# Kernel optimization log

Measured on AMD Instinct MI355X. Metric: run time of the kernel, lower is better.

The kernel has to match this reference:

```python
import jax, jax.numpy as jnp
import numpy as np

MEM, W, K = 65536, 128, 8
R = K + 1  # sparse reads + last-used slot
B, IN = 32, 512
IFACE = 2 * W + R + 1  # 266


def setup_inputs() -> dict:
    key = jax.random.key(0)
    ks = jax.random.split(key, 8)
    return {
        "x": jax.random.normal(ks[0], (B, IN), jnp.float32),
        "W_if": jax.random.normal(ks[1], (IN, IFACE), jnp.float32) * 0.02,
        "b_if": jnp.zeros((IFACE,), jnp.float32),
        "memory": jax.random.normal(ks[2], (B, MEM, W), jnp.float32),
        "read_weights": jax.random.uniform(ks[3], (B, 1, R), jnp.float32),
        "read_vectors": jax.random.normal(ks[4], (B, R, W), jnp.float32),
        "read_positions": jax.random.randint(ks[5], (B, R), 0, MEM, jnp.int32),
        "last_used_mem": jax.random.randint(ks[6], (B, 1), 0, MEM, jnp.int32),
    }


def reference(x, W_if, b_if, memory, read_weights, read_vectors, read_positions, last_used_mem):
    b = x.shape[0]
    # interface projection (independent_linears=False path)
    xi = x @ W_if + b_if                                   # (b, 2w+r+1)
    read_query = xi[:, :W]                                  # (b, w)
    write_vector = xi[:, W:2 * W][:, None, :]               # (b, 1, w)
    gate = jax.nn.sigmoid(xi[:, 2 * W:2 * W + R])[:, None, :]  # (b, 1, r)
    write_gate = jax.nn.sigmoid(xi[:, -1])[:, None, None]   # (b, 1, 1)
    # write: interpolate read weights, outer-product update of read vectors
    write_weights = write_gate * (gate * read_weights + (1.0 - gate))  # (b,1,r)
    new_rv = read_vectors + jnp.einsum('bkr,bkw->brw', write_weights, write_vector)  # (b,r,w)
    # write_into_sparse_memory: scatter read vectors into previous read positions
    brange = jnp.arange(b)[:, None]
    memory = memory.at[brange, read_positions].set(new_rv)
    # read: exact KNN (replaces CPU KD-tree search): squared L2 to all cells
    d2 = (jnp.sum(memory * memory, axis=-1)
          - 2.0 * jnp.einsum('bmw,bw->bm', memory, read_query)
          + jnp.sum(read_query * read_query, axis=-1, keepdims=True))  # (b, m)
    _, pos = jax.lax.top_k(-d2, K)                          # K nearest positions
    positions = jnp.concatenate([jnp.clip(pos, 0, MEM - 1), last_used_mem], axis=1)  # (b, r)
    gathered = jnp.take_along_axis(memory, positions[:, :, None], axis=1)  # (b, r, w)
    return gathered[:, :-1, :]  # (b, K, w) — forward output of read()
```

## Files before the change

### kernel.cpp

```cpp
#include <hip/hip_runtime.h>
#include <float.h>
#include <limits.h>

#define MEMN 65536
#define WD 128
#define KSEL 8
#define RD 9
#define BD 32
#define IND 512
#define IFACE 266
#define XI_STRIDE 272

#define KSEG 8
#define KSEG_LEN (IND / KSEG)

#define NCHUNK 64
#define ROWS_PER_CHUNK 1024
#define CAND_SCAN (NCHUNK * KSEL)
#define CAND_REAL (CAND_SCAN + RD)
#define CAND_PER_BATCH 528

typedef float fvec4 __attribute__((ext_vector_type(4)));

#define TOP8_INSERT(bv, bi, vin, iin)                                  \
  { float _v = (vin); int _i = (iin);                                  \
    _Pragma("unroll")                                                  \
    for (int _j = 0; _j < 8; ++_j) {                                   \
      bool _b = (_v < bv[_j]) || (_v == bv[_j] && _i < bi[_j]);        \
      float _tv = bv[_j]; int _ti = bi[_j];                            \
      bv[_j] = _b ? _v : _tv;  bi[_j] = _b ? _i : _ti;                 \
      _v = _b ? _tv : _v;      _i = _b ? _ti : _i;                     \
    } }

__device__ __forceinline__ fvec4 ntload(const void* p) {
  return __builtin_nontemporal_load((const fvec4*)p);
}

__global__ __launch_bounds__(288)
void xi_part_kernel(const float* __restrict__ x, const float* __restrict__ Wif,
                    float* __restrict__ xi_part) {
  const int b = blockIdx.x, seg = blockIdx.y, c = threadIdx.x;
  if (c >= IFACE) return;
  const float* xr = x + b * IND + seg * KSEG_LEN;
  const float* wp = Wif + (size_t)(seg * KSEG_LEN) * IFACE + c;
  float a0 = 0.f, a1 = 0.f, a2 = 0.f, a3 = 0.f;
  #pragma unroll
  for (int k = 0; k < KSEG_LEN; k += 4) {
    a0 += xr[k]     * wp[(size_t)k * IFACE];
    a1 += xr[k + 1] * wp[(size_t)(k + 1) * IFACE];
    a2 += xr[k + 2] * wp[(size_t)(k + 2) * IFACE];
    a3 += xr[k + 3] * wp[(size_t)(k + 3) * IFACE];
  }
  xi_part[(b * KSEG + seg) * XI_STRIDE + c] = (a0 + a1) + (a2 + a3);
}

__global__ __launch_bounds__(320)
void head_kernel(const float* __restrict__ xi_part, const float* __restrict__ bif,
                 const float* __restrict__ read_weights, const float* __restrict__ read_vectors,
                 const int* __restrict__ rpos,
                 float* __restrict__ xi, float* __restrict__ new_rv,
                 float* __restrict__ cand_val, int* __restrict__ cand_idx) {
  const int b = blockIdx.x, t = threadIdx.x;
  __shared__ float xiS[IFACE];
  __shared__ float wwS[RD];
  __shared__ float nvS[RD][WD];

  if (t < IFACE) {
    float acc = bif[t];
    #pragma unroll
    for (int s = 0; s < KSEG; ++s)
      acc += xi_part[(b * KSEG + s) * XI_STRIDE + t];
    xiS[t] = acc;
    xi[b * XI_STRIDE + t] = acc;
  }
  __syncthreads();

  if (t < RD) {
    float g  = 1.f / (1.f + __expf(-xiS[2 * WD + t]));
    float wg = 1.f / (1.f + __expf(-xiS[IFACE - 1]));
    wwS[t] = wg * (g * read_weights[b * RD + t] + (1.f - g));
  }
  __syncthreads();

  if (t < WD) {
    const float wv = xiS[WD + t];
    #pragma unroll
    for (int r = 0; r < RD; ++r) {
      float nv = read_vectors[(b * RD + r) * WD + t] + wwS[r] * wv;
      nvS[r][t] = nv;
      new_rv[(b * RD + r) * WD + t] = nv;
    }
  }
  __syncthreads();

  if (t < 64) {
    const int lane = t;
    const float q0 = xiS[lane * 2], q1 = xiS[lane * 2 + 1];
    for (int r = 0; r < RD; ++r) {
      float m0 = nvS[r][lane * 2], m1 = nvS[r][lane * 2 + 1];
      float s = m0 * (m0 - 2.f * q0) + m1 * (m1 - 2.f * q1);
      #pragma unroll
      for (int off = 32; off; off >>= 1) s += __shfl_xor(s, off);
      if (lane == 0) {
        int p = rpos[b * RD + r];
        bool dup = false;
        for (int r2 = r + 1; r2 < RD; ++r2) dup |= (rpos[b * RD + r2] == p);
        int slot = b * CAND_PER_BATCH + CAND_SCAN + r;
        cand_val[slot] = dup ? FLT_MAX : s;
        cand_idx[slot] = dup ? INT_MAX : p;
      }
    }
  }
}

__global__ __launch_bounds__(256)
void scan_kernel(const float* __restrict__ memory, const float* __restrict__ xi,
                 const int* __restrict__ rpos,
                 float* __restrict__ cand_val, int* __restrict__ cand_idx) {
  const int b = blockIdx.y, chunk = blockIdx.x;
  const int t = threadIdx.x;
  const int w = t >> 6, l = t & 63, g = l >> 2, ln = l & 3;
  const int chunkBase = chunk * ROWS_PER_CHUNK;

  int rp[RD];
  #pragma unroll
  for (int r = 0; r < RD; ++r) rp[r] = rpos[b * RD + r];

  fvec4 tq[8];
  #pragma unroll
  for (int j = 0; j < 8; ++j) {
    fvec4 q = *(const fvec4*)(xi + b * XI_STRIDE + j * 16 + ln * 4);
    tq[j] = q * 2.f;
  }

  float bv[8]; int bi[8];
  #pragma unroll
  for (int j = 0; j < 8; ++j) { bv[j] = FLT_MAX; bi[j] = INT_MAX; }

  const char* memB = (const char*)memory + (size_t)b * MEMN * (WD * 4);

  #pragma unroll 2
  for (int i = 0; i < ROWS_PER_CHUNK / 64; ++i) {
    const int m = chunkBase + i * 64 + w * 16 + g;
    const char* p = memB + (size_t)m * (WD * 4) + ln * 16;
    float sA = 0.f, sB = 0.f;
    #pragma unroll
    for (int j = 0; j < 8; j += 2) {
      fvec4 m0 = ntload(p + j * 64);
      fvec4 m1 = ntload(p + (j + 1) * 64);
      sA += m0.x * (m0.x - tq[j].x) + m0.y * (m0.y - tq[j].y)
          + m0.z * (m0.z - tq[j].z) + m0.w * (m0.w - tq[j].w);
      sB += m1.x * (m1.x - tq[j + 1].x) + m1.y * (m1.y - tq[j + 1].y)
          + m1.z * (m1.z - tq[j + 1].z) + m1.w * (m1.w - tq[j + 1].w);
    }
    float s = sA + sB;
    s += __shfl_xor(s, 1);
    s += __shfl_xor(s, 2);
    if (ln == 0) {
      bool skip = false;
      #pragma unroll
      for (int r = 0; r < RD; ++r) skip |= (m == rp[r]);
      if (!skip && (s < bv[7] || (s == bv[7] && m < bi[7]))) TOP8_INSERT(bv, bi, s, m);
    }
  }

  __shared__ float lv[64][8];
  __shared__ int   li[64][8];
  if (ln == 0) {
    #pragma unroll
    for (int j = 0; j < 8; ++j) { lv[w * 16 + g][j] = bv[j]; li[w * 16 + g][j] = bi[j]; }
  }
  __syncthreads();
  for (int s = 32; s >= 1; s >>= 1) {
    if (t < s) {
      float mv[8]; int mi[8];
      #pragma unroll
      for (int j = 0; j < 8; ++j) { mv[j] = lv[t][j]; mi[j] = li[t][j]; }
      #pragma unroll
      for (int j = 0; j < 8; ++j) {
        float v = lv[t + s][j]; int i = li[t + s][j];
        if (v < mv[7] || (v == mv[7] && i < mi[7])) TOP8_INSERT(mv, mi, v, i);
      }
      #pragma unroll
      for (int j = 0; j < 8; ++j) { lv[t][j] = mv[j]; li[t][j] = mi[j]; }
    }
    __syncthreads();
  }
  if (t < 8) {
    cand_val[b * CAND_PER_BATCH + chunk * 8 + t] = lv[0][t];
    cand_idx[b * CAND_PER_BATCH + chunk * 8 + t] = li[0][t];
  }
}

__global__ __launch_bounds__(128)
void final_kernel(const float* __restrict__ cand_val, const int* __restrict__ cand_idx,
                  const float* __restrict__ memory, const float* __restrict__ new_rv,
                  const int* __restrict__ rpos, float* __restrict__ out) {
  const int b = blockIdx.x, t = threadIdx.x;
  __shared__ float lv[128][8];
  __shared__ int   li[128][8];
  __shared__ int   posS[KSEL], srcS[KSEL];

  float bv[8]; int bi[8];
  #pragma unroll
  for (int j = 0; j < 8; ++j) { bv[j] = FLT_MAX; bi[j] = INT_MAX; }

  for (int e = t; e < CAND_REAL; e += 128) {
    float v = cand_val[b * CAND_PER_BATCH + e];
    int   i = cand_idx[b * CAND_PER_BATCH + e];
    if (v < bv[7] || (v == bv[7] && i < bi[7])) TOP8_INSERT(bv, bi, v, i);
  }
  #pragma unroll
  for (int j = 0; j < 8; ++j) { lv[t][j] = bv[j]; li[t][j] = bi[j]; }
  __syncthreads();

  for (int stride = 64; stride >= 1; stride >>= 1) {
    if (t < stride) {
      #pragma unroll
      for (int j = 0; j < 8; ++j) {
        float v = lv[t + stride][j]; int i = li[t + stride][j];
        if (v < bv[7] || (v == bv[7] && i < bi[7])) TOP8_INSERT(bv, bi, v, i);
      }
      #pragma unroll
      for (int j = 0; j < 8; ++j) { lv[t][j] = bv[j]; li[t][j] = bi[j]; }
    }
    __syncthreads();
  }

  if (t < KSEL) {
    int p = li[0][t];
    int src = -1;
    for (int r = 0; r < RD; ++r) if (rpos[b * RD + r] == p) src = r;
    posS[t] = p; srcS[t] = src;
  }
  __syncthreads();

  for (int e = t; e < KSEL * WD; e += 128) {
    int k = e >> 7, w = e & 127;
    int p = posS[k], src = srcS[k];
    float val = (src >= 0) ? new_rv[(b * RD + src) * WD + w]
                           : memory[((size_t)b * MEMN + p) * WD + w];
    out[b * KSEL * WD + e] = val;
  }
}

extern "C" void kernel_launch(void* const* d_in, const int* in_sizes, int n_in,
                              void* d_out, int out_size, void* d_ws, size_t ws_size,
                              hipStream_t stream) {
  const float* x      = (const float*)d_in[0];
  const float* Wif    = (const float*)d_in[1];
  const float* bif    = (const float*)d_in[2];
  const float* memory = (const float*)d_in[3];
  const float* rw     = (const float*)d_in[4];
  const float* rv     = (const float*)d_in[5];
  const int*   rpos   = (const int*)d_in[6];

  float* ws       = (float*)d_ws;
  float* xi_part  = ws;
  float* xi       = xi_part + BD * KSEG * XI_STRIDE;
  float* new_rv   = xi + BD * XI_STRIDE;
  float* cand_val = new_rv + BD * RD * WD;
  int*   cand_idx = (int*)(cand_val + BD * CAND_PER_BATCH);
  float* out      = (float*)d_out;

  xi_part_kernel<<<dim3(BD, KSEG), dim3(288), 0, stream>>>(x, Wif, xi_part);
  head_kernel<<<dim3(BD), dim3(320), 0, stream>>>(xi_part, bif, rw, rv, rpos,
                                                  xi, new_rv, cand_val, cand_idx);
  scan_kernel<<<dim3(NCHUNK, BD), dim3(256), 0, stream>>>(memory, xi, rpos, cand_val, cand_idx);
  final_kernel<<<dim3(BD), dim3(128), 0, stream>>>(cand_val, cand_idx, memory, new_rv, rpos, out);
}
```

Baseline: 241.7 us.

## Fuse interface projection into head kernel and remap scan to half-wave rows

The separate xi_part kernel is removed, and the x·W_if projection now runs inside head_kernel, split across two 272-thread halves. This drops one launch and a global round trip. The scan kernel changes from 4 lanes per row to 32 lanes per row, with each half-wave reading one contiguous 512-byte row. Each thread holds 4 rows per iteration, and the shared-memory top-8 merge shrinks from 64 to 8 partial lists. Nontemporal loads are replaced with plain loads, and the head projection now runs on only 32 blocks, which limits its parallelism.

```diff
diff --git a/kernel.cpp b/kernel.cpp
--- a/kernel.cpp
+++ b/kernel.cpp
@@ -10,9 +10,6 @@
 #define IND 512
 #define IFACE 266
 #define XI_STRIDE 272
-
-#define KSEG 8
-#define KSEG_LEN (IND / KSEG)
 
 #define NCHUNK 64
 #define ROWS_PER_CHUNK 1024
@@ -32,44 +29,37 @@
       _v = _b ? _tv : _v;      _i = _b ? _ti : _i;                     \
     } }
 
-__device__ __forceinline__ fvec4 ntload(const void* p) {
-  return __builtin_nontemporal_load((const fvec4*)p);
-}
-
-__global__ __launch_bounds__(288)
-void xi_part_kernel(const float* __restrict__ x, const float* __restrict__ Wif,
-                    float* __restrict__ xi_part) {
-  const int b = blockIdx.x, seg = blockIdx.y, c = threadIdx.x;
-  if (c >= IFACE) return;
-  const float* xr = x + b * IND + seg * KSEG_LEN;
-  const float* wp = Wif + (size_t)(seg * KSEG_LEN) * IFACE + c;
-  float a0 = 0.f, a1 = 0.f, a2 = 0.f, a3 = 0.f;
-  #pragma unroll
-  for (int k = 0; k < KSEG_LEN; k += 4) {
-    a0 += xr[k]     * wp[(size_t)k * IFACE];
-    a1 += xr[k + 1] * wp[(size_t)(k + 1) * IFACE];
-    a2 += xr[k + 2] * wp[(size_t)(k + 2) * IFACE];
-    a3 += xr[k + 3] * wp[(size_t)(k + 3) * IFACE];
-  }
-  xi_part[(b * KSEG + seg) * XI_STRIDE + c] = (a0 + a1) + (a2 + a3);
-}
-
-__global__ __launch_bounds__(320)
-void head_kernel(const float* __restrict__ xi_part, const float* __restrict__ bif,
+__global__ __launch_bounds__(544)
+void head_kernel(const float* __restrict__ x, const float* __restrict__ Wif,
+                 const float* __restrict__ bif,
                  const float* __restrict__ read_weights, const float* __restrict__ read_vectors,
                  const int* __restrict__ rpos,
                  float* __restrict__ xi, float* __restrict__ new_rv,
                  float* __restrict__ cand_val, int* __restrict__ cand_idx) {
   const int b = blockIdx.x, t = threadIdx.x;
+  __shared__ float part[2][272];
   __shared__ float xiS[IFACE];
   __shared__ float wwS[RD];
   __shared__ float nvS[RD][WD];
 
+  const int c = t % 272, h = t / 272;
+  if (c < IFACE) {
+    const float* xr = x + b * IND + h * 256;
+    const float* wp = Wif + (size_t)(h * 256) * IFACE + c;
+    float a0 = 0.f, a1 = 0.f, a2 = 0.f, a3 = 0.f;
+    #pragma unroll 4
+    for (int k = 0; k < 256; k += 4) {
+      a0 += xr[k]     * wp[(k)     * IFACE];
+      a1 += xr[k + 1] * wp[(k + 1) * IFACE];
+      a2 += xr[k + 2] * wp[(k + 2) * IFACE];
+      a3 += xr[k + 3] * wp[(k + 3) * IFACE];
+    }
+    part[h][c] = (a0 + a1) + (a2 + a3);
+  }
+  __syncthreads();
+
   if (t < IFACE) {
-    float acc = bif[t];
-    #pragma unroll
-    for (int s = 0; s < KSEG; ++s)
-      acc += xi_part[(b * KSEG + s) * XI_STRIDE + t];
+    float acc = bif[t] + part[0][t] + part[1][t];
     xiS[t] = acc;
     xi[b * XI_STRIDE + t] = acc;
   }
@@ -119,59 +109,68 @@
                  float* __restrict__ cand_val, int* __restrict__ cand_idx) {
   const int b = blockIdx.y, chunk = blockIdx.x;
   const int t = threadIdx.x;
-  const int w = t >> 6, l = t & 63, g = l >> 2, ln = l & 3;
-  const int chunkBase = chunk * ROWS_PER_CHUNK;
+  const int w = t >> 6, l = t & 63;
+  const int half = l >> 5;
+  const int waveBase = chunk * ROWS_PER_CHUNK + w * (ROWS_PER_CHUNK / 4);
 
   int rp[RD];
   #pragma unroll
   for (int r = 0; r < RD; ++r) rp[r] = rpos[b * RD + r];
 
-  fvec4 tq[8];
-  #pragma unroll
-  for (int j = 0; j < 8; ++j) {
-    fvec4 q = *(const fvec4*)(xi + b * XI_STRIDE + j * 16 + ln * 4);
-    tq[j] = q * 2.f;
-  }
+  const fvec4 q = *(const fvec4*)(xi + b * XI_STRIDE + (l & 31) * 4);
+  const fvec4 tq = q * 2.f;
 
   float bv[8]; int bi[8];
   #pragma unroll
   for (int j = 0; j < 8; ++j) { bv[j] = FLT_MAX; bi[j] = INT_MAX; }
 
-  const char* memB = (const char*)memory + (size_t)b * MEMN * (WD * 4);
+  const char* base = (const char*)memory
+                   + ((size_t)b * MEMN + waveBase) * (WD * 4) + (size_t)l * 16;
 
   #pragma unroll 2
-  for (int i = 0; i < ROWS_PER_CHUNK / 64; ++i) {
-    const int m = chunkBase + i * 64 + w * 16 + g;
-    const char* p = memB + (size_t)m * (WD * 4) + ln * 16;
-    float sA = 0.f, sB = 0.f;
+  for (int i = 0; i < 32; ++i) {
+    const char* p = base + (size_t)i * 4096;
+    const fvec4 m0 = *(const fvec4*)(p);
+    const fvec4 m1 = *(const fvec4*)(p + 1024);
+    const fvec4 m2 = *(const fvec4*)(p + 2048);
+    const fvec4 m3 = *(const fvec4*)(p + 3072);
+
+    float s0 = m0.x*(m0.x-tq.x) + m0.y*(m0.y-tq.y) + m0.z*(m0.z-tq.z) + m0.w*(m0.w-tq.w);
+    float s1 = m1.x*(m1.x-tq.x) + m1.y*(m1.y-tq.y) + m1.z*(m1.z-tq.z) + m1.w*(m1.w-tq.w);
+    float s2 = m2.x*(m2.x-tq.x) + m2.y*(m2.y-tq.y) + m2.z*(m2.z-tq.z) + m2.w*(m2.w-tq.w);
+    float s3 = m3.x*(m3.x-tq.x) + m3.y*(m3.y-tq.y) + m3.z*(m3.z-tq.z) + m3.w*(m3.w-tq.w);
+
     #pragma unroll
-    for (int j = 0; j < 8; j += 2) {
-      fvec4 m0 = ntload(p + j * 64);
-      fvec4 m1 = ntload(p + (j + 1) * 64);
-      sA += m0.x * (m0.x - tq[j].x) + m0.y * (m0.y - tq[j].y)
-          + m0.z * (m0.z - tq[j].z) + m0.w * (m0.w - tq[j].w);
-      sB += m1.x * (m1.x - tq[j + 1].x) + m1.y * (m1.y - tq[j + 1].y)
-          + m1.z * (m1.z - tq[j + 1].z) + m1.w * (m1.w - tq[j + 1].w);
-    }
-    float s = sA + sB;
-    s += __shfl_xor(s, 1);
-    s += __shfl_xor(s, 2);
-    if (ln == 0) {
-      bool skip = false;
-      #pragma unroll
-      for (int r = 0; r < RD; ++r) skip |= (m == rp[r]);
-      if (!skip && (s < bv[7] || (s == bv[7] && m < bi[7]))) TOP8_INSERT(bv, bi, s, m);
-    }
-  }
-
-  __shared__ float lv[64][8];
-  __shared__ int   li[64][8];
-  if (ln == 0) {
+    for (int off = 1; off < 32; off <<= 1) {
+      s0 += __shfl_xor(s0, off);
+      s1 += __shfl_xor(s1, off);
+      s2 += __shfl_xor(s2, off);
+      s3 += __shfl_xor(s3, off);
+    }
+
+    if ((l & 31) == 0) {
+      const int mr = waveBase + i * 8 + half;
+      bool k0 = false, k1 = false, k2 = false, k3 = false;
+      #pragma unroll
+      for (int r = 0; r < RD; ++r) {
+        k0 |= (mr     == rp[r]); k1 |= (mr + 2 == rp[r]);
+        k2 |= (mr + 4 == rp[r]); k3 |= (mr + 6 == rp[r]);
+      }
+      if (!k0 && (s0 < bv[7] || (s0 == bv[7] && mr     < bi[7]))) TOP8_INSERT(bv, bi, s0, mr);
+      if (!k1 && (s1 < bv[7] || (s1 == bv[7] && mr + 2 < bi[7]))) TOP8_INSERT(bv, bi, s1, mr + 2);
+      if (!k2 && (s2 < bv[7] || (s2 == bv[7] && mr + 4 < bi[7]))) TOP8_INSERT(bv, bi, s2, mr + 4);
+      if (!k3 && (s3 < bv[7] || (s3 == bv[7] && mr + 6 < bi[7]))) TOP8_INSERT(bv, bi, s3, mr + 6);
+    }
+  }
+
+  __shared__ float lv[8][8];
+  __shared__ int   li[8][8];
+  if ((l & 31) == 0) {
     #pragma unroll
-    for (int j = 0; j < 8; ++j) { lv[w * 16 + g][j] = bv[j]; li[w * 16 + g][j] = bi[j]; }
-  }
-  __syncthreads();
-  for (int s = 32; s >= 1; s >>= 1) {
+    for (int j = 0; j < 8; ++j) { lv[w * 2 + half][j] = bv[j]; li[w * 2 + half][j] = bi[j]; }
+  }
+  __syncthreads();
+  for (int s = 4; s >= 1; s >>= 1) {
     if (t < s) {
       float mv[8]; int mi[8];
       #pragma unroll
@@ -236,10 +235,10 @@
   __syncthreads();
 
   for (int e = t; e < KSEL * WD; e += 128) {
-    int k = e >> 7, w = e & 127;
+    int k = e >> 7, wv = e & 127;
     int p = posS[k], src = srcS[k];
-    float val = (src >= 0) ? new_rv[(b * RD + src) * WD + w]
-                           : memory[((size_t)b * MEMN + p) * WD + w];
+    float val = (src >= 0) ? new_rv[(b * RD + src) * WD + wv]
+                           : memory[((size_t)b * MEMN + p) * WD + wv];
     out[b * KSEL * WD + e] = val;
   }
 }
@@ -256,15 +255,13 @@
   const int*   rpos   = (const int*)d_in[6];
 
   float* ws       = (float*)d_ws;
-  float* xi_part  = ws;
-  float* xi       = xi_part + BD * KSEG * XI_STRIDE;
+  float* xi       = ws;
   float* new_rv   = xi + BD * XI_STRIDE;
   float* cand_val = new_rv + BD * RD * WD;
   int*   cand_idx = (int*)(cand_val + BD * CAND_PER_BATCH);
   float* out      = (float*)d_out;
 
-  xi_part_kernel<<<dim3(BD, KSEG), dim3(288), 0, stream>>>(x, Wif, xi_part);
-  head_kernel<<<dim3(BD), dim3(320), 0, stream>>>(xi_part, bif, rw, rv, rpos,
+  head_kernel<<<dim3(BD), dim3(544), 0, stream>>>(x, Wif, bif, rw, rv, rpos,
                                                   xi, new_rv, cand_val, cand_idx);
   scan_kernel<<<dim3(NCHUNK, BD), dim3(256), 0, stream>>>(memory, xi, rpos, cand_val, cand_idx);
   final_kernel<<<dim3(BD), dim3(128), 0, stream>>>(cand_val, cand_idx, memory, new_rv, rpos, out);
```

After: 254.0 us. +5.1%, slower.
